# Kernel optimization log

Hardware: AMD Instinct MI355X
Metric: run time of the kernel (lower is better)

Reference implementation:

```python
import jax, jax.numpy as jnp
import numpy as np

T, B, I, H, O = 2048, 128, 128, 512, 128


def setup_inputs() -> dict:
    key = jax.random.key(0)
    ks = jax.random.split(key, 8)
    s = 0.05  # keep tanh out of hard saturation
    return {
        "input_seq": jax.random.randint(ks[0], (T, B), 0, I),
        "emb": jax.random.normal(ks[1], (I, I), jnp.float32),
        "Wxh_w": jax.random.normal(ks[2], (H, I), jnp.float32) * s,
        "Wxh_b": jax.random.normal(ks[3], (H,), jnp.float32) * s,
        "Whh_w": jax.random.normal(ks[4], (H, H), jnp.float32) * s,
        "Whh_b": jax.random.normal(ks[5], (H,), jnp.float32) * s,
        "dec_w": jax.random.normal(ks[6], (O, H), jnp.float32) * s,
        "dec_b": jax.random.normal(ks[7], (O,), jnp.float32) * s,
    }


def reference(input_seq, emb, Wxh_w, Wxh_b, Whh_w, Whh_b, dec_w, dec_b):
    x = emb[input_seq]                                   # [T, B, I]
    # input projection is h-independent: hoist out of the recurrence
    xh = jnp.einsum("tbi,hi->tbh", x, Wxh_w) + Wxh_b    # [T, B, H]

    def step(h, xt):
        # torch: res = tanh(Whh(h) + Wxh(x1)); self.h = res.detach()
        res = jnp.tanh(h @ Whh_w.T + Whh_b + xt)         # [B, H]
        return jax.lax.stop_gradient(res), res

    h0 = jnp.zeros((x.shape[1], Whh_w.shape[0]), x.dtype)
    _, out = jax.lax.scan(step, h0, xh)                  # [T, B, H]
    return out @ dec_w.T + dec_b                         # [T, B, O]
```

## Files before the change

### kernel.cpp

```cpp
#include <hip/hip_runtime.h>


#define TT 2048
#define BB 128
#define HH 512
#define OO 128
#define MAGIC 123456.0f
#define NVG 184
#define NLD 56
#define NST 16

typedef _Float16 h2_t __attribute__((ext_vector_type(2)));
union UF { unsigned int u; float f; h2_t h; unsigned short us[2]; };

__device__ __forceinline__ unsigned int packf16(float a, float b) {
  UF r; r.h[0] = (_Float16)a; r.h[1] = (_Float16)b; return r.u;
}
__device__ __forceinline__ float dot2a(unsigned int a, unsigned int b, float c) {
  UF x, y; x.u = a; y.u = b;
#if __has_builtin(__builtin_amdgcn_fdot2)
  return __builtin_amdgcn_fdot2(x.h, y.h, c, false);
#else
  return fmaf((float)x.h[1], (float)y.h[1], fmaf((float)x.h[0], (float)y.h[0], c));
#endif
}
__device__ __forceinline__ unsigned short f16bits(float x) {
  UF r; r.h[0] = (_Float16)x; r.h[1] = (_Float16)0.f; return r.us[0];
}
__device__ __forceinline__ float tanh_fast(float x) {
  float e = __expf(2.0f * x);
  return 1.0f - 2.0f / (e + 1.0f);
}
__device__ __forceinline__ float sanz(float x) {
  return (x >= -1e20f && x <= 1e20f) ? x : 0.f;
}

extern "C" __global__ void k_init(float* __restrict__ mk) {
  if (threadIdx.x < 8) mk[threadIdx.x] = 0.f;
}

extern "C" __global__ __launch_bounds__(512)
void k_pre(const float* __restrict__ emb, const float* __restrict__ wxh,
           const float* __restrict__ bxh, const float* __restrict__ bhh,
           float* __restrict__ P, float* __restrict__ mk) {
  const int id = blockIdx.x;
  const int j = threadIdx.x;
  const float4* er = (const float4*)(emb + id * 128);
  const float4* wr = (const float4*)(wxh + j * 128);
  float acc = 0.f;
  #pragma unroll
  for (int c = 0; c < 32; ++c) {
    const float4 e = er[c], w = wr[c];
    acc = fmaf(e.x, w.x, fmaf(e.y, w.y, fmaf(e.z, w.z, fmaf(e.w, w.w, acc))));
  }
  P[id * HH + j] = acc + bxh[j] + bhh[j];
  if (id == 0 && j == 0) mk[0] = MAGIC;
}

extern "C" __global__ __launch_bounds__(256)
void k_pack(const float* __restrict__ whh, unsigned int* __restrict__ wpack) {
  const int row = blockIdx.x;
  const int pd = threadIdx.x;
  const float2 w = *(const float2*)(whh + row * 512 + 2 * pd);
  wpack[row * 256 + pd] = packf16(w.x, w.y);
}

extern "C" __global__ __launch_bounds__(512)
void k_pack2(const float* __restrict__ whh, uint4* __restrict__ wst4) {
  const int q = blockIdx.x;
  const int t = threadIdx.x;
  const float* src = whh + t * 512 + 480 + 8 * q;
  uint4 v;
  v.x = packf16(src[0], src[1]);
  v.y = packf16(src[2], src[3]);
  v.z = packf16(src[4], src[5]);
  v.w = packf16(src[6], src[7]);
  wst4[q * 512 + t] = v;
}

extern "C" __global__ __launch_bounds__(512, 2)
void k_rec(const int* __restrict__ idx, const float* __restrict__ P,
           const unsigned int* __restrict__ wpack, const uint4* __restrict__ wst4,
           float* __restrict__ hstate, float* __restrict__ ring,
           float* __restrict__ mk, int t0, int nT) {
  extern __shared__ __align__(16) unsigned int smem[];
  unsigned int* wl = smem;
  unsigned int* hb32 = smem + NLD * 512;
  unsigned short* hb16 = (unsigned short*)hb32;
  const int tid = threadIdx.x;
  const int b = blockIdx.x;
  if (t0 == 0 && b == 0 && tid == 0) mk[1] = MAGIC;

  unsigned int wreg[NVG];
  {
    const uint4* wp = (const uint4*)(wpack + tid * 256);
    #pragma unroll
    for (int q = 0; q < NVG / 4; ++q) {
      const uint4 v = wp[q];
      wreg[4 * q + 0] = v.x; wreg[4 * q + 1] = v.y;
      wreg[4 * q + 2] = v.z; wreg[4 * q + 3] = v.w;
    }
    const unsigned int* ws = wpack + tid * 256 + NVG;
    #pragma unroll
    for (int s = 0; s < NLD; ++s) wl[s * 512 + tid] = ws[s];
  }
  const float h0 = (t0 == 0) ? 0.f : hstate[b * HH + tid];
  hb16[tid] = f16bits(h0);
  float hlast = h0;
  __syncthreads();

  for (int tl = 0; tl < nT; ++tl) {
    const int rb = tl & 1, wb = rb ^ 1;
    uint4 w4s[4];
    #pragma unroll
    for (int q = 0; q < 4; ++q) w4s[q] = wst4[q * 512 + tid];
    const int id = idx[(t0 + tl) * BB + b];
    const float pj = P[id * HH + tid];
    const unsigned int* h = hb32 + rb * 256;
    float acc = 0.f;
    #pragma unroll
    for (int c4 = 0; c4 < NVG / 4; ++c4) {
      const uint4 h4 = *(const uint4*)(h + 4 * c4);
      acc = dot2a(wreg[4 * c4 + 0], h4.x, acc);
      acc = dot2a(wreg[4 * c4 + 1], h4.y, acc);
      acc = dot2a(wreg[4 * c4 + 2], h4.z, acc);
      acc = dot2a(wreg[4 * c4 + 3], h4.w, acc);
    }
    #pragma unroll
    for (int j = 0; j < NLD / 4; ++j) {
      const uint4 h4 = *(const uint4*)(h + NVG + 4 * j);
      acc = dot2a(wl[(4 * j + 0) * 512 + tid], h4.x, acc);
      acc = dot2a(wl[(4 * j + 1) * 512 + tid], h4.y, acc);
      acc = dot2a(wl[(4 * j + 2) * 512 + tid], h4.z, acc);
      acc = dot2a(wl[(4 * j + 3) * 512 + tid], h4.w, acc);
    }
    #pragma unroll
    for (int q = 0; q < 4; ++q) {
      const uint4 h4 = *(const uint4*)(h + NVG + NLD + 4 * q);
      acc = dot2a(w4s[q].x, h4.x, acc);
      acc = dot2a(w4s[q].y, h4.y, acc);
      acc = dot2a(w4s[q].z, h4.z, acc);
      acc = dot2a(w4s[q].w, h4.w, acc);
    }
    float s = acc + pj;
    s = fminf(fmaxf(s, -30.f), 30.f);
    const float hv = tanh_fast(s);
    hb16[wb * 512 + tid] = f16bits(hv);
    ring[((size_t)tl * BB + b) * HH + tid] = hv;
    hlast = hv;
    __syncthreads();
  }
  hstate[b * HH + tid] = hlast;
  if (t0 == 0 && b == 0 && tid == 0) mk[2] = MAGIC;
}

extern "C" __global__ __launch_bounds__(256)
void k_dec(const float* __restrict__ ring, const float* __restrict__ dw,
           const float* __restrict__ decb, float* __restrict__ out,
           float* __restrict__ mk, int t0) {
  __shared__ float hl[32][132];
  const int tid = threadIdx.x;
  const size_t r0 = (size_t)blockIdx.x * 32;
  const int oq = tid & 31, tbq = tid >> 5;
  float acc[4][4];
  #pragma unroll
  for (int rI = 0; rI < 4; ++rI)
    #pragma unroll
    for (int s = 0; s < 4; ++s) acc[rI][s] = 0.f;

  for (int cb = 0; cb < 4; ++cb) {
    __syncthreads();
    #pragma unroll
    for (int i = 0; i < 16; ++i) {
      const int idx2 = i * 256 + tid;
      const int tb = idx2 >> 7, c = idx2 & 127;
      hl[tb][c] = ring[(r0 + tb) * HH + cb * 128 + c];
    }
    __syncthreads();
    #pragma unroll 2
    for (int cp2 = 0; cp2 < 32; ++cp2) {
      float4 h4[4];
      #pragma unroll
      for (int s = 0; s < 4; ++s) h4[s] = *(const float4*)&hl[tbq + s * 8][cp2 * 4];
      #pragma unroll
      for (int rI = 0; rI < 4; ++rI) {
        const int o = oq + rI * 32;
        const float4 w4 = *(const float4*)(dw + o * 512 + cb * 128 + cp2 * 4);
        #pragma unroll
        for (int s = 0; s < 4; ++s)
          acc[rI][s] = fmaf(w4.x, h4[s].x, fmaf(w4.y, h4[s].y,
                       fmaf(w4.z, h4[s].z, fmaf(w4.w, h4[s].w, acc[rI][s]))));
      }
    }
  }
  #pragma unroll
  for (int rI = 0; rI < 4; ++rI) {
    const int o = oq + rI * 32;
    const float db = decb[o];
    #pragma unroll
    for (int s = 0; s < 4; ++s)
      out[((size_t)t0 * BB + r0 + tbq + s * 8) * OO + o] = sanz(acc[rI][s] + db);
  }
  if (t0 == 0 && blockIdx.x == 0 && tid == 0) mk[3] = MAGIC;
}

extern "C" __global__ void k_probe(const float* __restrict__ mk, float* __restrict__ out,
                                   int wsTooSmall) {
  if (wsTooSmall)     { out[0] = 100000.f; return; }
  if (mk[0] != MAGIC) { out[0] = 200000.f; return; }
  if (mk[1] != MAGIC) { out[0] = 300000.f; return; }
  if (mk[2] != MAGIC) { out[0] = 400000.f; return; }
  if (mk[3] != MAGIC) { out[0] = 500000.f; return; }
}

extern "C" void kernel_launch(void* const* d_in, const int* in_sizes, int n_in,
                              void* d_out, int out_size, void* d_ws, size_t ws_size,
                              hipStream_t stream) {
  (void)in_sizes; (void)n_in; (void)out_size;
  const int* idx = (const int*)d_in[0];
  const float* emb = (const float*)d_in[1];
  const float* wxh = (const float*)d_in[2];
  const float* bxh = (const float*)d_in[3];
  const float* whh = (const float*)d_in[4];
  const float* bhh = (const float*)d_in[5];
  const float* dw  = (const float*)d_in[6];
  const float* db  = (const float*)d_in[7];
  float* out = (float*)d_out;

  char* ws = (char*)d_ws;
  float* P = (float*)ws;
  float* hstate = (float*)(ws + (256 << 10));
  float* mk = (float*)(ws + (512 << 10));
  unsigned int* wpack = (unsigned int*)(ws + (516 << 10));
  uint4* wst4 = (uint4*)(ws + (1028 << 10));
  float* ring = (float*)(ws + (1060 << 10));

  int chunkT = 0;
  const int opts[6] = {2048, 512, 128, 32, 8, 2};
  for (int i = 0; i < 6; ++i) {
    const size_t need = (size_t)(1060 << 10) + (size_t)opts[i] * BB * HH * 4;
    if (ws_size >= need) { chunkT = opts[i]; break; }
  }
  if (chunkT == 0) {
    k_probe<<<1, 1, 0, stream>>>(nullptr, out, 1);
    return;
  }

  const int ldsRec = (NLD * 512 + 512) * 4;
  (void)hipFuncSetAttribute(reinterpret_cast<const void*>(k_rec),
                            hipFuncAttributeMaxDynamicSharedMemorySize, ldsRec);

  k_init<<<1, 64, 0, stream>>>(mk);
  k_pre<<<128, 512, 0, stream>>>(emb, wxh, bxh, bhh, P, mk);
  k_pack<<<512, 256, 0, stream>>>(whh, wpack);
  k_pack2<<<4, 512, 0, stream>>>(whh, wst4);
  for (int t0 = 0; t0 < TT; t0 += chunkT) {
    k_rec<<<BB, 512, ldsRec, stream>>>(idx, P, wpack, wst4, hstate, ring, mk, t0, chunkT);
    k_dec<<<chunkT * 4, 256, 0, stream>>>(ring, dw, db, out, mk, t0);
  }
  k_probe<<<1, 1, 0, stream>>>(mk, out, 0);
}
```

Measured before the change: 5.624 ms.

## Broadcast hidden state via readlane, store fp16 ring, fp16 packed decoder

The recurrence kernel now loads one uint4 of the fp16 hidden state per lane and broadcasts it across the wave with readlane, instead of having every thread read the full hidden vector from LDS. Weights are held as uint4 groups split between registers, LDS and streamed global loads, and four accumulators break the dependency chain. The hidden-state ring is stored in fp16 to halve its traffic. The decoder uses fp16 packed weights with dot2 and loads its 64-row tile into LDS once. Readlane serialization and the larger register footprint could limit gains, and fp16 ring storage lowers decoder input precision.

```diff
diff --git a/kernel.cpp b/kernel.cpp
--- a/kernel.cpp
+++ b/kernel.cpp
@@ -6,9 +6,9 @@
 #define HH 512
 #define OO 128
 #define MAGIC 123456.0f
-#define NVG 184
-#define NLD 56
-#define NST 16
+#define NVP 43
+#define NLD 15
+#define NSTR 6
 
 typedef _Float16 h2_t __attribute__((ext_vector_type(2)));
 union UF { unsigned int u; float f; h2_t h; unsigned short us[2]; };
@@ -33,6 +33,13 @@
 }
 __device__ __forceinline__ float sanz(float x) {
   return (x >= -1e20f && x <= 1e20f) ? x : 0.f;
+}
+__device__ __forceinline__ unsigned int rdlane(unsigned int v, int l) {
+#if __has_builtin(__builtin_amdgcn_readlane)
+  return (unsigned int)__builtin_amdgcn_readlane((int)v, l);
+#else
+  return (unsigned int)__shfl((int)v, l, 64);
+#endif
 }
 
 extern "C" __global__ void k_init(float* __restrict__ mk) {
@@ -66,43 +73,65 @@
 }
 
 extern "C" __global__ __launch_bounds__(512)
-void k_pack2(const float* __restrict__ whh, uint4* __restrict__ wst4) {
+void k_pack3(const float* __restrict__ whh, uint4* __restrict__ wstr4) {
   const int q = blockIdx.x;
   const int t = threadIdx.x;
-  const float* src = whh + t * 512 + 480 + 8 * q;
+  const float* src = whh + t * 512 + 464 + 8 * q;
   uint4 v;
   v.x = packf16(src[0], src[1]);
   v.y = packf16(src[2], src[3]);
   v.z = packf16(src[4], src[5]);
   v.w = packf16(src[6], src[7]);
-  wst4[q * 512 + t] = v;
-}
-
-extern "C" __global__ __launch_bounds__(512, 2)
+  wstr4[q * 512 + t] = v;
+}
+
+extern "C" __global__ __launch_bounds__(256)
+void k_packd(const float* __restrict__ dw, uint4* __restrict__ decP4) {
+  const int id = blockIdx.x * 256 + threadIdx.x;
+  const int c4 = id >> 7, o = id & 127;
+  const float* src = dw + o * 512 + 8 * c4;
+  uint4 v;
+  v.x = packf16(src[0], src[1]);
+  v.y = packf16(src[2], src[3]);
+  v.z = packf16(src[4], src[5]);
+  v.w = packf16(src[6], src[7]);
+  decP4[id] = v;
+}
+
+#define GSTEP(W4, g)                                              \
+  {                                                               \
+    const unsigned int bc0 = rdlane(hv.x, (g));                   \
+    const unsigned int bc1 = rdlane(hv.y, (g));                   \
+    const unsigned int bc2 = rdlane(hv.z, (g));                   \
+    const unsigned int bc3 = rdlane(hv.w, (g));                   \
+    a0 = dot2a((W4).x, bc0, a0);                                  \
+    a1 = dot2a((W4).y, bc1, a1);                                  \
+    a2 = dot2a((W4).z, bc2, a2);                                  \
+    a3 = dot2a((W4).w, bc3, a3);                                  \
+  }
+
+extern "C" __global__
+__attribute__((amdgpu_flat_work_group_size(512, 512), amdgpu_waves_per_eu(2, 2)))
 void k_rec(const int* __restrict__ idx, const float* __restrict__ P,
-           const unsigned int* __restrict__ wpack, const uint4* __restrict__ wst4,
-           float* __restrict__ hstate, float* __restrict__ ring,
+           const unsigned int* __restrict__ wpack, const uint4* __restrict__ wstr4,
+           float* __restrict__ hstate, unsigned short* __restrict__ ring16,
            float* __restrict__ mk, int t0, int nT) {
-  extern __shared__ __align__(16) unsigned int smem[];
-  unsigned int* wl = smem;
-  unsigned int* hb32 = smem + NLD * 512;
-  unsigned short* hb16 = (unsigned short*)hb32;
+  extern __shared__ __align__(16) unsigned char smem[];
+  uint4* wl4 = (uint4*)smem;
+  unsigned short* hb16 = (unsigned short*)(smem + NLD * 512 * 16);
+  const uint4* hb4 = (const uint4*)hb16;
   const int tid = threadIdx.x;
   const int b = blockIdx.x;
+  const int lane = tid & 63;
   if (t0 == 0 && b == 0 && tid == 0) mk[1] = MAGIC;
 
-  unsigned int wreg[NVG];
+  uint4 wreg[NVP];
   {
-    const uint4* wp = (const uint4*)(wpack + tid * 256);
-    #pragma unroll
-    for (int q = 0; q < NVG / 4; ++q) {
-      const uint4 v = wp[q];
-      wreg[4 * q + 0] = v.x; wreg[4 * q + 1] = v.y;
-      wreg[4 * q + 2] = v.z; wreg[4 * q + 3] = v.w;
-    }
-    const unsigned int* ws = wpack + tid * 256 + NVG;
-    #pragma unroll
-    for (int s = 0; s < NLD; ++s) wl[s * 512 + tid] = ws[s];
+    const uint4* wp = (const uint4*)(wpack + (size_t)tid * 256);
+    #pragma unroll
+    for (int q = 0; q < NVP; ++q) wreg[q] = wp[q];
+    #pragma unroll
+    for (int s = 0; s < NLD; ++s) wl4[s * 512 + tid] = wp[NVP + s];
   }
   const float h0 = (t0 == 0) ? 0.f : hstate[b * HH + tid];
   hb16[tid] = f16bits(h0);
@@ -110,96 +139,83 @@
   __syncthreads();
 
   for (int tl = 0; tl < nT; ++tl) {
+    asm volatile("" ::: "memory");
     const int rb = tl & 1, wb = rb ^ 1;
-    uint4 w4s[4];
-    #pragma unroll
-    for (int q = 0; q < 4; ++q) w4s[q] = wst4[q * 512 + tid];
+    uint4 st[NSTR];
+    #pragma unroll
+    for (int q = 0; q < NSTR; ++q) st[q] = wstr4[q * 512 + tid];
     const int id = idx[(t0 + tl) * BB + b];
     const float pj = P[id * HH + tid];
-    const unsigned int* h = hb32 + rb * 256;
-    float acc = 0.f;
-    #pragma unroll
-    for (int c4 = 0; c4 < NVG / 4; ++c4) {
-      const uint4 h4 = *(const uint4*)(h + 4 * c4);
-      acc = dot2a(wreg[4 * c4 + 0], h4.x, acc);
-      acc = dot2a(wreg[4 * c4 + 1], h4.y, acc);
-      acc = dot2a(wreg[4 * c4 + 2], h4.z, acc);
-      acc = dot2a(wreg[4 * c4 + 3], h4.w, acc);
+    const uint4 hv = hb4[rb * 64 + lane];
+    float a0 = 0.f, a1 = 0.f, a2 = 0.f, a3 = 0.f;
+    #pragma unroll
+    for (int g = 0; g < NVP; ++g) GSTEP(wreg[g], g);
+    #pragma unroll
+    for (int g2 = 0; g2 < NLD; ++g2) {
+      const uint4 w4 = wl4[g2 * 512 + tid];
+      GSTEP(w4, NVP + g2);
     }
     #pragma unroll
-    for (int j = 0; j < NLD / 4; ++j) {
-      const uint4 h4 = *(const uint4*)(h + NVG + 4 * j);
-      acc = dot2a(wl[(4 * j + 0) * 512 + tid], h4.x, acc);
-      acc = dot2a(wl[(4 * j + 1) * 512 + tid], h4.y, acc);
-      acc = dot2a(wl[(4 * j + 2) * 512 + tid], h4.z, acc);
-      acc = dot2a(wl[(4 * j + 3) * 512 + tid], h4.w, acc);
-    }
-    #pragma unroll
-    for (int q = 0; q < 4; ++q) {
-      const uint4 h4 = *(const uint4*)(h + NVG + NLD + 4 * q);
-      acc = dot2a(w4s[q].x, h4.x, acc);
-      acc = dot2a(w4s[q].y, h4.y, acc);
-      acc = dot2a(w4s[q].z, h4.z, acc);
-      acc = dot2a(w4s[q].w, h4.w, acc);
-    }
-    float s = acc + pj;
+    for (int q = 0; q < NSTR; ++q) GSTEP(st[q], NVP + NLD + q);
+    float s = a0 + a1 + a2 + a3 + pj;
     s = fminf(fmaxf(s, -30.f), 30.f);
-    const float hv = tanh_fast(s);
-    hb16[wb * 512 + tid] = f16bits(hv);
-    ring[((size_t)tl * BB + b) * HH + tid] = hv;
-    hlast = hv;
+    const float hvf = tanh_fast(s);
+    const unsigned short h16 = f16bits(hvf);
+    hb16[wb * 512 + tid] = h16;
+    ring16[((size_t)tl * BB + b) * HH + tid] = h16;
+    hlast = hvf;
     __syncthreads();
   }
   hstate[b * HH + tid] = hlast;
   if (t0 == 0 && b == 0 && tid == 0) mk[2] = MAGIC;
 }
 
-extern "C" __global__ __launch_bounds__(256)
-void k_dec(const float* __restrict__ ring, const float* __restrict__ dw,
+extern "C" __global__ __launch_bounds__(512)
+void k_dec(const uint4* __restrict__ ring4, const uint4* __restrict__ decP4,
            const float* __restrict__ decb, float* __restrict__ out,
            float* __restrict__ mk, int t0) {
-  __shared__ float hl[32][132];
+  extern __shared__ __align__(16) unsigned char smem[];
+  uint4* hl4 = (uint4*)smem;
   const int tid = threadIdx.x;
-  const size_t r0 = (size_t)blockIdx.x * 32;
-  const int oq = tid & 31, tbq = tid >> 5;
+  const size_t r0 = (size_t)blockIdx.x * 64;
+  #pragma unroll
+  for (int i = 0; i < 8; ++i) {
+    const int u = i * 512 + tid;
+    const int row = u >> 6, c4 = u & 63;
+    hl4[u] = ring4[(r0 + row) * 64 + c4];
+  }
+  __syncthreads();
+  const int oq = tid & 31, tq = tid >> 5;
   float acc[4][4];
   #pragma unroll
-  for (int rI = 0; rI < 4; ++rI)
-    #pragma unroll
-    for (int s = 0; s < 4; ++s) acc[rI][s] = 0.f;
-
-  for (int cb = 0; cb < 4; ++cb) {
-    __syncthreads();
-    #pragma unroll
-    for (int i = 0; i < 16; ++i) {
-      const int idx2 = i * 256 + tid;
-      const int tb = idx2 >> 7, c = idx2 & 127;
-      hl[tb][c] = ring[(r0 + tb) * HH + cb * 128 + c];
+  for (int r = 0; r < 4; ++r)
+    #pragma unroll
+    for (int s = 0; s < 4; ++s) acc[r][s] = 0.f;
+  #pragma unroll 2
+  for (int c4 = 0; c4 < 64; ++c4) {
+    uint4 h4[4], d4[4];
+    #pragma unroll
+    for (int s = 0; s < 4; ++s) h4[s] = hl4[(tq + 16 * s) * 64 + c4];
+    #pragma unroll
+    for (int r = 0; r < 4; ++r) d4[r] = decP4[c4 * 128 + oq + 32 * r];
+    #pragma unroll
+    for (int r = 0; r < 4; ++r)
+      #pragma unroll
+      for (int s = 0; s < 4; ++s) {
+        acc[r][s] = dot2a(d4[r].x, h4[s].x, acc[r][s]);
+        acc[r][s] = dot2a(d4[r].y, h4[s].y, acc[r][s]);
+        acc[r][s] = dot2a(d4[r].z, h4[s].z, acc[r][s]);
+        acc[r][s] = dot2a(d4[r].w, h4[s].w, acc[r][s]);
+      }
+  }
+  #pragma unroll
+  for (int r = 0; r < 4; ++r) {
+    const float db = decb[oq + 32 * r];
+    #pragma unroll
+    for (int s = 0; s < 4; ++s) {
+      const size_t g = r0 + tq + 16 * s;
+      out[((size_t)t0 * BB + g) * OO + oq + 32 * r] = sanz(acc[r][s] + db);
     }
-    __syncthreads();
-    #pragma unroll 2
-    for (int cp2 = 0; cp2 < 32; ++cp2) {
-      float4 h4[4];
-      #pragma unroll
-      for (int s = 0; s < 4; ++s) h4[s] = *(const float4*)&hl[tbq + s * 8][cp2 * 4];
-      #pragma unroll
-      for (int rI = 0; rI < 4; ++rI) {
-        const int o = oq + rI * 32;
-        const float4 w4 = *(const float4*)(dw + o * 512 + cb * 128 + cp2 * 4);
-        #pragma unroll
-        for (int s = 0; s < 4; ++s)
-          acc[rI][s] = fmaf(w4.x, h4[s].x, fmaf(w4.y, h4[s].y,
-                       fmaf(w4.z, h4[s].z, fmaf(w4.w, h4[s].w, acc[rI][s]))));
-      }
-    }
-  }
-  #pragma unroll
-  for (int rI = 0; rI < 4; ++rI) {
-    const int o = oq + rI * 32;
-    const float db = decb[o];
-    #pragma unroll
-    for (int s = 0; s < 4; ++s)
-      out[((size_t)t0 * BB + r0 + tbq + s * 8) * OO + o] = sanz(acc[rI][s] + db);
   }
   if (t0 == 0 && blockIdx.x == 0 && tid == 0) mk[3] = MAGIC;
 }
@@ -232,13 +248,14 @@
   float* hstate = (float*)(ws + (256 << 10));
   float* mk = (float*)(ws + (512 << 10));
   unsigned int* wpack = (unsigned int*)(ws + (516 << 10));
-  uint4* wst4 = (uint4*)(ws + (1028 << 10));
-  float* ring = (float*)(ws + (1060 << 10));
+  uint4* wstr4 = (uint4*)(ws + (1028 << 10));
+  uint4* decP4 = (uint4*)(ws + (1076 << 10));
+  unsigned short* ring16 = (unsigned short*)(ws + (1204 << 10));
 
   int chunkT = 0;
-  const int opts[6] = {2048, 512, 128, 32, 8, 2};
-  for (int i = 0; i < 6; ++i) {
-    const size_t need = (size_t)(1060 << 10) + (size_t)opts[i] * BB * HH * 4;
+  const int opts[8] = {2048, 1024, 768, 512, 256, 128, 32, 8};
+  for (int i = 0; i < 8; ++i) {
+    const size_t need = (size_t)(1204 << 10) + (size_t)opts[i] * BB * HH * 2;
     if (ws_size >= need) { chunkT = opts[i]; break; }
   }
   if (chunkT == 0) {
@@ -246,17 +263,21 @@
     return;
   }
 
-  const int ldsRec = (NLD * 512 + 512) * 4;
+  const int ldsRec = NLD * 512 * 16 + 2048;
+  const int ldsDec = 64 * 64 * 16;
   (void)hipFuncSetAttribute(reinterpret_cast<const void*>(k_rec),
                             hipFuncAttributeMaxDynamicSharedMemorySize, ldsRec);
+  (void)hipFuncSetAttribute(reinterpret_cast<const void*>(k_dec),
+                            hipFuncAttributeMaxDynamicSharedMemorySize, ldsDec);
 
   k_init<<<1, 64, 0, stream>>>(mk);
   k_pre<<<128, 512, 0, stream>>>(emb, wxh, bxh, bhh, P, mk);
   k_pack<<<512, 256, 0, stream>>>(whh, wpack);
-  k_pack2<<<4, 512, 0, stream>>>(whh, wst4);
+  k_pack3<<<6, 512, 0, stream>>>(whh, wstr4);
+  k_packd<<<32, 256, 0, stream>>>(dw, decP4);
   for (int t0 = 0; t0 < TT; t0 += chunkT) {
-    k_rec<<<BB, 512, ldsRec, stream>>>(idx, P, wpack, wst4, hstate, ring, mk, t0, chunkT);
-    k_dec<<<chunkT * 4, 256, 0, stream>>>(ring, dw, db, out, mk, t0);
+    k_rec<<<BB, 512, ldsRec, stream>>>(idx, P, wpack, wstr4, hstate, ring16, mk, t0, chunkT);
+    k_dec<<<chunkT * 2, 512, ldsDec, stream>>>((const uint4*)ring16, decP4, db, out, mk, t0);
   }
   k_probe<<<1, 1, 0, stream>>>(mk, out, 0);
 }
```

Measured after the change: 5.156 ms. 8.3% less time.
